# Optimization experiments

Measured on AMD Instinct MI355X. Metric: run time of the kernel, lower is better.

Reference implementation:

```python
import jax, jax.numpy as jnp
import numpy as np

B, TE, TD, EH, DH = 128, 512, 128, 512, 512
K_CNN, C_CNN = 7, 105

def setup_inputs() -> dict:
    key = jax.random.key(0)
    ks = jax.random.split(key, 20)
    n = lambda k, shp: jax.random.normal(k, shp, dtype=jnp.float32) * 0.05
    return {
        "LSTM": jax.random.normal(ks[0], (B, TE, EH), dtype=jnp.float32),
        "CNNs": jax.random.normal(ks[1], (B, K_CNN, C_CNN), dtype=jnp.float32),
        "Wa_w": n(ks[2], (TD, DH)), "Wa_b": n(ks[3], (TD,)),
        "Ua_w": n(ks[4], (TE, EH)), "Ua_b": n(ks[5], (TE,)),
        "va_w": n(ks[6], (1, TE + TD)), "va_b": n(ks[7], (1,)),
        "phi_w": n(ks[8], (EH, TE)), "phi_b": n(ks[9], (EH,)),
        "Wih": n(ks[10], (4 * DH, C_CNN + EH)), "Whh": n(ks[11], (4 * DH, DH)),
        "bih": n(ks[12], (4 * DH,)), "bhh": n(ks[13], (4 * DH,)),
        "wij_w": n(ks[14], (K_CNN, DH + C_CNN)), "wij_b": n(ks[15], (K_CNN,)),
        "s_i": jax.random.uniform(ks[16], (B, DH), dtype=jnp.float32),
        "m_i": jax.random.uniform(ks[17], (B, DH), dtype=jnp.float32),
    }

def reference(LSTM, CNNs, Wa_w, Wa_b, Ua_w, Ua_b, va_w, va_b, phi_w, phi_b,
              Wih, Whh, bih, bhh, wij_w, wij_b, s_i, m_i):
    Bn, Te, Eh = LSTM.shape
    Td = Wa_w.shape[0]
    Dh = s_i.shape[1]
    # delta_i_j for all j: strict lower-triangular one-hots [Te, Te]
    Dm = jnp.tril(jnp.ones((Te, Te), LSTM.dtype), k=-1)
    phi = Dm @ phi_w.T + phi_b                     # [Te, Eh]
    ph = phi[None, :, :] * LSTM                    # [B, Te, Eh] phi_delta * LSTM[:, j]
    Ua = jnp.einsum('bte,se->bts', ph, Ua_w) + Ua_b  # [B, Te, Te]
    Wa = s_i @ Wa_w.T + Wa_b                       # [B, Td] (same for all i, j)
    cat = jnp.concatenate([jnp.broadcast_to(Wa[:, None, :], (Bn, Te, Td)), Ua], axis=-1)
    Cw = jnp.tanh(cat) * va_w[0]                   # [B, Te, Td+Te]
    # one-hot mask picks index i + Te - j; v_a reduces to a single gathered term + bias
    idx = jnp.arange(Td)[:, None] + Te - jnp.arange(Te)[None, :]   # [Td, Te]
    e = Cw[:, jnp.arange(Te)[None, :], idx] + va_b[0]              # [B, Td, Te]
    a = jax.nn.softmax(e, axis=-1)
    c_i = jnp.einsum('bit,bte->bie', a, LSTM)      # [B, Td, Eh]
    # CNN attention (same for all decoder steps; note non-standard normalizer kept faithfully)
    w_cnn, w_s = wij_w[:, :C_CNN], wij_w[:, C_CNN:]
    ep = jnp.tanh(jnp.einsum('bkc,kc->bk', CNNs, w_cnn) + s_i @ w_s.T + wij_b)  # [B, K]
    ap = jnp.exp(ep) / jnp.sum(ep)
    c_p = jnp.einsum('bk,bkc->bc', ap, CNNs)       # [B, C_CNN]
    # LSTMCell with fixed (s_i, m_i) state => all decoder steps vectorize over i
    x = jnp.concatenate([c_i, jnp.broadcast_to(c_p[:, None, :], (Bn, Td, C_CNN))], axis=-1)
    gates = jnp.einsum('bid,gd->big', x, Wih) + bih + (s_i @ Whh.T + bhh)[:, None, :]
    ig, fg, gg, og = jnp.split(gates, 4, axis=-1)
    cnew = jax.nn.sigmoid(fg) * m_i[:, None, :] + jax.nn.sigmoid(ig) * jnp.tanh(gg)
    h = jax.nn.sigmoid(og) * jnp.tanh(cnew)        # [B, Td, Dh]
    return h
```

## Files before the change

kernel.cpp:

```cpp
#include <hip/hip_runtime.h>
#include <hip/hip_bf16.h>

#define B_   128
#define TE_  512
#define TD_  128
#define EH_  512
#define DH_  512
#define KC_  7
#define CC_  105
#define G_   2048
#define KX_  617
#define KP_  640
#define GNT  10

typedef __attribute__((ext_vector_type(8))) short bf16x8;
typedef __attribute__((ext_vector_type(4))) float f32x4;

__device__ __forceinline__ float sigm(float x){ return 1.f/(1.f + __expf(-x)); }
__device__ __forceinline__ float tanhf_fast(float x){
  float e = __expf(2.f*x);
  return 1.f - 2.f/(e + 1.f);
}

__device__ __forceinline__ unsigned short f2bf(float f){
  unsigned int u = __float_as_uint(f);
  unsigned int r = (u + 0x7fffu + ((u >> 16) & 1u)) >> 16;
  return (unsigned short)r;
}

typedef __attribute__((address_space(3))) unsigned int lds_u32_t;
typedef __attribute__((address_space(1))) const unsigned int glb_u32_t;
__device__ __forceinline__ void gload16(const void* g, void* l) {
  __builtin_amdgcn_global_load_lds((glb_u32_t*)g, (lds_u32_t*)l, 16, 0, 0);
}

static const size_t OFF_PHI  = 0;
static const size_t OFF_WA   = OFF_PHI  + (size_t)TE_*EH_*4;
static const size_t OFF_HPRE = OFF_WA   + (size_t)B_*TD_*4;
static const size_t OFF_EP   = OFF_HPRE + (size_t)B_*G_*4;
static const size_t OFF_CP   = OFF_EP   + 4096;
static const size_t OFF_ET   = ((OFF_CP + (size_t)B_*CC_*4 + 255)/256)*256;
static const size_t OFF_STAT = OFF_ET + (size_t)B_*TE_*TD_*4;
static const size_t OFF_P    = ((OFF_STAT + (size_t)2*B_*TD_*4 + 255)/256)*256;
static const size_t OFF_LT   = OFF_P  + (size_t)B_*TD_*TE_*2;
static const size_t OFF_WR   = OFF_LT + (size_t)B_*TE_*EH_*2;
static const size_t OFF_SP   = OFF_WR + (size_t)G_*KP_*2;
static const size_t OFF_PT   = OFF_P;
static const size_t OFF_SUM  = OFF_PT + (size_t)TE_*EH_*4;
static const size_t OFF_WT   = OFF_P + (size_t)2*1024*1024;
static const size_t OFF_WAT  = OFF_P + (size_t)6*1024*1024;

__global__ __launch_bounds__(256) void k_tr(const float* __restrict__ src,
                                            float* __restrict__ dst, int R, int C) {
  int r0 = blockIdx.x * 64, c0 = blockIdx.y * 64;
  __shared__ float tile[64][65];
  int tid = threadIdx.x;
  int r = tid >> 2, c16 = (tid & 3) * 16;
  const float4* s4 = (const float4*)(src + (size_t)(r0 + r)*C + c0 + c16);
  float4 v0 = s4[0], v1 = s4[1], v2 = s4[2], v3 = s4[3];
  *(float4*)&tile[r][c16]    = v0;
  *(float4*)&tile[r][c16+4]  = v1;
  *(float4*)&tile[r][c16+8]  = v2;
  *(float4*)&tile[r][c16+12] = v3;
  __syncthreads();
  float o[16];
  #pragma unroll
  for (int j = 0; j < 16; ++j) o[j] = tile[c16+j][r];
  float* d = dst + (size_t)(c0 + r)*R + r0 + c16;
  *(float4*)d      = *(float4*)&o[0];
  *(float4*)(d+4)  = *(float4*)&o[4];
  *(float4*)(d+8)  = *(float4*)&o[8];
  *(float4*)(d+12) = *(float4*)&o[12];
}

__global__ void k_phiA(const float* __restrict__ phiT, float* __restrict__ phi,
                       float* __restrict__ sums) {
  int e = blockIdx.x * 256 + threadIdx.x;
  int z = blockIdx.y;
  float acc = 0.f;
  for (int t = z*64; t < z*64 + 64; ++t) {
    phi[(size_t)t*EH_ + e] = acc;
    acc += phiT[(size_t)t*EH_ + e];
  }
  sums[z*EH_ + e] = acc;
}
__global__ void k_phiB(const float* __restrict__ sums, const float* __restrict__ phi_b,
                       float* __restrict__ phi) {
  int e = blockIdx.x * 256 + threadIdx.x;
  int z = blockIdx.y;
  float off = phi_b[e];
  for (int zz = 0; zz < z; ++zz) off += sums[zz*EH_ + e];
  for (int t = z*64; t < z*64 + 64; ++t)
    phi[(size_t)t*EH_ + e] += off;
}

__global__ __launch_bounds__(256) void k_wa2(const float* __restrict__ s_i,
                                             const float* __restrict__ WaT,
                                             const float* __restrict__ Wa_b,
                                             const float* __restrict__ va_w,
                                             float* __restrict__ wa) {
  int lane = threadIdx.x & 63, wv = threadIdx.x >> 6;
  int b = blockIdx.x * 4 + wv;
  int d0 = lane * 2;
  const float2* w = (const float2*)WaT + lane;
  const float* s = s_i + (size_t)b*DH_;
  float ax = 0.f, ay = 0.f;
  #pragma unroll 8
  for (int k = 0; k < DH_; ++k) {
    float2 wv2 = w[(size_t)k*64];
    float x = s[k];
    ax += wv2.x * x; ay += wv2.y * x;
  }
  wa[b*TD_ + d0]     = tanhf_fast(ax + Wa_b[d0])     * va_w[d0];
  wa[b*TD_ + d0 + 1] = tanhf_fast(ay + Wa_b[d0 + 1]) * va_w[d0 + 1];
}

__global__ __launch_bounds__(256) void k_hpre2(const float* __restrict__ s_i,
                                               const float* __restrict__ WhhT,
                                               const float* __restrict__ bih,
                                               const float* __restrict__ bhh,
                                               float* __restrict__ hpre) {
  int gq = blockIdx.x * 256 + threadIdx.x;
  int b  = blockIdx.y;
  const float4* w = (const float4*)WhhT + gq;
  const float* s = s_i + (size_t)b*DH_;
  float4 a = {0.f,0.f,0.f,0.f};
  #pragma unroll 8
  for (int k = 0; k < DH_; ++k) {
    float4 wv = w[(size_t)k*512];
    float x = s[k];
    a.x += wv.x*x; a.y += wv.y*x; a.z += wv.z*x; a.w += wv.w*x;
  }
  int g = gq * 4;
  float4 bi = *(const float4*)(bih + g);
  float4 bh = *(const float4*)(bhh + g);
  float4 o;
  o.x = a.x + bi.x + bh.x; o.y = a.y + bi.y + bh.y;
  o.z = a.z + bi.z + bh.z; o.w = a.w + bi.w + bh.w;
  *(float4*)(hpre + (size_t)b*G_ + g) = o;
}

__global__ __launch_bounds__(256) void k_ep(const float* __restrict__ CNNs,
                                            const float* __restrict__ wij_w,
                                            const float* __restrict__ wij_b,
                                            const float* __restrict__ s_i,
                                            float* __restrict__ ep) {
  int gw = blockIdx.x * 4 + (threadIdx.x >> 6);
  int lane = threadIdx.x & 63;
  if (gw >= B_*KC_) return;
  int b = gw / KC_, k = gw % KC_;
  const float* cr = CNNs + (size_t)(b*KC_ + k)*CC_;
  const float* wr = wij_w + (size_t)k*KX_;
  float acc = 0.f;
  for (int c = lane; c < CC_; c += 64) acc += cr[c] * wr[c];
  const float* sr = s_i + (size_t)b*DH_;
  const float* wsr = wr + CC_;
  #pragma unroll
  for (int j = 0; j < 8; ++j) { int h = lane + j*64; acc += sr[h] * wsr[h]; }
  #pragma unroll
  for (int m = 32; m; m >>= 1) acc += __shfl_xor(acc, m, 64);
  if (lane == 0) ep[gw] = tanhf_fast(acc + wij_b[k]);
}

__global__ void k_epsum(const float* __restrict__ ep, float* __restrict__ epsum) {
  __shared__ float red[1024];
  int tid = threadIdx.x;
  red[tid] = (tid < B_*KC_) ? ep[tid] : 0.f;
  __syncthreads();
  for (int off = 512; off > 0; off >>= 1) {
    if (tid < off) red[tid] += red[tid + off];
    __syncthreads();
  }
  if (tid == 0) epsum[0] = red[0];
}

__global__ __launch_bounds__(128) void k_cp(const float* __restrict__ ep,
                                            const float* __restrict__ epsum,
                                            const float* __restrict__ CNNs,
                                            unsigned short* __restrict__ X) {
  int b = blockIdx.x, c = threadIdx.x;
  float S = epsum[0];
  float apl[KC_];
  #pragma unroll
  for (int k = 0; k < KC_; ++k) apl[k] = __expf(ep[b*KC_ + k]) / S;
  float acc = 0.f;
  if (c < CC_) {
    #pragma unroll
    for (int k = 0; k < KC_; ++k)
      acc += apl[k] * CNNs[(size_t)(b*KC_ + k)*CC_ + c];
  }
  unsigned short o = (c < CC_) ? f2bf(acc) : 0;
  unsigned short* xb = X + (size_t)b*TD_*KP_ + EH_ + c;
  for (int i = 0; i < TD_; ++i)
    xb[(size_t)i*KP_] = o;
}

__global__ void k_cvtW(const float* __restrict__ Wih, unsigned short* __restrict__ Wr) {
  int id = blockIdx.x * 256 + threadIdx.x;
  int nr = id / 80, c8 = (id % 80) * 8;
  int gate = nr & 3, dh = nr >> 2;
  const float* src = Wih + (size_t)(gate*DH_ + dh)*KX_;
  unsigned short o[8];
  #pragma unroll
  for (int j = 0; j < 8; ++j) {
    int col = c8 + j;
    o[j] = (col < KX_) ? f2bf(src[col]) : 0;
  }
  *(uint4*)(Wr + (size_t)nr*KP_ + c8) = *(uint4*)o;
}

__global__ __launch_bounds__(256) void k_ltrans(const float* __restrict__ LSTM,
                                                unsigned short* __restrict__ LT) {
  int e0 = blockIdx.x * 64, t0 = blockIdx.y * 64, b = blockIdx.z;
  __shared__ float tile[64][65];
  int tid = threadIdx.x;
  int tt = tid >> 2, c16 = (tid & 3) * 16;
  const float4* src = (const float4*)(LSTM + ((size_t)b*TE_ + t0 + tt)*EH_ + e0 + c16);
  float4 v0 = src[0], v1 = src[1], v2 = src[2], v3 = src[3];
  *(float4*)&tile[tt][c16]    = v0;
  *(float4*)&tile[tt][c16+4]  = v1;
  *(float4*)&tile[tt][c16+8]  = v2;
  *(float4*)&tile[tt][c16+12] = v3;
  __syncthreads();
  int e = tid >> 2, t16 = (tid & 3) * 16;
  unsigned short o[16];
  #pragma unroll
  for (int j = 0; j < 16; ++j) o[j] = f2bf(tile[t16+j][e]);
  unsigned short* dst = LT + ((size_t)b*EH_ + e0 + e)*TE_ + t0 + t16;
  *(uint4*)dst     = *(uint4*)&o[0];
  *(uint4*)(dst+8) = *(uint4*)&o[8];
}

#define BMM_M 64
#define LDA_  40
#define LDB_  40
#define OTS_  132
__global__ __launch_bounds__(256) void k_bandmm(const float* __restrict__ LSTM,
                                                const float* __restrict__ phi,
                                                const float* __restrict__ Ua_w,
                                                const float* __restrict__ Ua_b,
                                                const float* __restrict__ va_w,
                                                const float* __restrict__ va_b,
                                                const float* __restrict__ wa,
                                                unsigned short* __restrict__ P,
                                                float* __restrict__ sums_p) {
  int t0 = blockIdx.x * BMM_M;
  int b  = blockIdx.y;
  int s_base = 321 - t0;
  __shared__ __align__(16) char smem[BMM_M * OTS_ * 4];
  short* sA = (short*)smem;
  short* sB = (short*)(smem + BMM_M*LDA_*2);
  int tid = threadIdx.x;
  int wave = tid >> 6, lane = tid & 63;
  int quad = lane >> 4, l16 = lane & 15;

  f32x4 acc[4][3];
  #pragma unroll
  for (int m = 0; m < 4; ++m)
    #pragma unroll
    for (int n = 0; n < 3; ++n)
      acc[m][n] = (f32x4){0.f, 0.f, 0.f, 0.f};

  int arow = tid >> 2;
  int ach  = (tid & 3) * 8;
  int aq   = ach >> 2;

  const float4* baseL = (const float4*)(LSTM + ((size_t)b*TE_ + t0 + arow)*EH_);
  const float4* baseP = (const float4*)(phi + (size_t)(t0 + arow)*EH_);
  const float4* baseU[3];
  int brow[3], bch[3];
  #pragma unroll
  for (int c = 0; c < 3; ++c) {
    int idx = c*256 + tid;
    brow[c] = idx >> 2;
    bch[c]  = (idx & 3) * 8;
    int s = s_base + brow[c];
    int sc = s < 0 ? 0 : (s > 511 ? 511 : s);
    baseU[c] = (const float4*)(Ua_w + (size_t)sc*EH_ + bch[c]);
  }

  float4 l0 = baseL[aq], l1 = baseL[aq+1], p0 = baseP[aq], p1 = baseP[aq+1];
  float4 u0[3], u1[3];
  #pragma unroll
  for (int c = 0; c < 3; ++c) { u0[c] = baseU[c][0]; u1[c] = baseU[c][1]; }

  for (int k0 = 0; k0 < EH_; k0 += 32) {
    unsigned short at[8];
    at[0]=f2bf(l0.x*p0.x); at[1]=f2bf(l0.y*p0.y); at[2]=f2bf(l0.z*p0.z); at[3]=f2bf(l0.w*p0.w);
    at[4]=f2bf(l1.x*p1.x); at[5]=f2bf(l1.y*p1.y); at[6]=f2bf(l1.z*p1.z); at[7]=f2bf(l1.w*p1.w);
    unsigned short bt[3][8];
    #pragma unroll
    for (int c = 0; c < 3; ++c) {
      bt[c][0]=f2bf(u0[c].x); bt[c][1]=f2bf(u0[c].y); bt[c][2]=f2bf(u0[c].z); bt[c][3]=f2bf(u0[c].w);
      bt[c][4]=f2bf(u1[c].x); bt[c][5]=f2bf(u1[c].y); bt[c][6]=f2bf(u1[c].z); bt[c][7]=f2bf(u1[c].w);
    }
    if (k0 + 32 < EH_) {
      int q = (k0 + 32) >> 2;
      l0 = baseL[q+aq]; l1 = baseL[q+aq+1]; p0 = baseP[q+aq]; p1 = baseP[q+aq+1];
      #pragma unroll
      for (int c = 0; c < 3; ++c) { u0[c] = baseU[c][q]; u1[c] = baseU[c][q+1]; }
    }
    __syncthreads();
    *(uint4*)&sA[arow*LDA_ + ach] = *(uint4*)at;
    #pragma unroll
    for (int c = 0; c < 3; ++c)
      *(uint4*)&sB[brow[c]*LDB_ + bch[c]] = *(uint4*)bt[c];
    __syncthreads();
    bf16x8 bfr[3];
    #pragma unroll
    for (int n = 0; n < 3; ++n)
      bfr[n] = *(const bf16x8*)&sB[(l16 + (wave*3 + n)*16)*LDB_ + quad*8];
    #pragma unroll
    for (int m = 0; m < 4; ++m) {
      bf16x8 af = *(const bf16x8*)&sA[(l16 + m*16)*LDA_ + quad*8];
      #pragma unroll
      for (int n = 0; n < 3; ++n)
        acc[m][n] = __builtin_amdgcn_mfma_f32_16x16x32_bf16(af, bfr[n], acc[m][n], 0, 0, 0);
    }
  }

  __syncthreads();
  float* tileO = (float*)smem;
  float vb = va_b[0];
  #pragma unroll
  for (int n = 0; n < 3; ++n) {
    int s = s_base + wave*48 + n*16 + l16;
    float ub = (s >= 0 && s < TE_) ? Ua_b[s] : 0.f;
    float vw = (s >= 0 && s < TE_) ? va_w[TD_ + s] : 0.f;
    #pragma unroll
    for (int m = 0; m < 4; ++m) {
      #pragma unroll
      for (int r = 0; r < 4; ++r) {
        int tl = m*16 + quad*4 + r;
        int i = s + t0 + tl - 384;
        if (i >= 0 && i < TD_) {
          float val;
          if (s >= 0) val = tanhf_fast(acc[m][n][r] + ub) * vw + vb;
          else        val = wa[b*TD_ + s + 128] + vb;
          tileO[tl*OTS_ + i] = __expf(val);
        }
      }
    }
  }
  __syncthreads();
  if (tid < TD_) {
    float ssum = 0.f;
    #pragma unroll 8
    for (int tl = 0; tl < 64; ++tl) ssum += tileO[tl*OTS_ + tid];
    sums_p[((size_t)b*8 + blockIdx.x)*TD_ + tid] = ssum;
  }
  {
    int ii = tid >> 1, hf = tid & 1;
    unsigned short o[32];
    #pragma unroll
    for (int j = 0; j < 32; ++j)
      o[j] = f2bf(tileO[(hf*32 + j)*OTS_ + ii]);
    unsigned short* dst = P + ((size_t)b*TD_ + ii)*TE_ + t0 + hf*32;
    *(uint4*)dst      = *(uint4*)&o[0];
    *(uint4*)(dst+8)  = *(uint4*)&o[8];
    *(uint4*)(dst+16) = *(uint4*)&o[16];
    *(uint4*)(dst+24) = *(uint4*)&o[24];
  }
}

__global__ __launch_bounds__(128) void k_sinv(const float* __restrict__ sums_p,
                                              float* __restrict__ sinv) {
  int b = blockIdx.x, i = threadIdx.x;
  float s = 0.f;
  #pragma unroll
  for (int z = 0; z < 8; ++z) s += sums_p[((size_t)b*8 + z)*TD_ + i];
  sinv[b*TD_ + i] = 1.f / s;
}

#define CI_LD 40
__global__ __launch_bounds__(256) void k_ci_mm(const unsigned short* __restrict__ P,
                                               const unsigned short* __restrict__ LT,
                                               const float* __restrict__ sinv,
                                               unsigned short* __restrict__ X) {
  int b = blockIdx.x, e0 = blockIdx.y * 128;
  __shared__ short sA[128 * CI_LD];
  __shared__ short sB[128 * CI_LD];
  int tid = threadIdx.x;
  int wave = tid >> 6, lane = tid & 63, quad = lane >> 4, l16 = lane & 15;
  int wm = wave >> 1, wn = wave & 1;
  int row = tid >> 1, ho = (tid & 1) * 16;

  const unsigned short* pa = P + ((size_t)b*TD_ + row)*TE_ + ho;
  const unsigned short* pb = LT + ((size_t)b*EH_ + e0 + row)*TE_ + ho;

  f32x4 acc[4][4];
  #pragma unroll
  for (int m = 0; m < 4; ++m)
    #pragma unroll
    for (int n = 0; n < 4; ++n)
      acc[m][n] = (f32x4){0.f, 0.f, 0.f, 0.f};

  uint4 a0 = *(const uint4*)pa, a1 = *(const uint4*)(pa + 8);
  uint4 b0 = *(const uint4*)pb, b1 = *(const uint4*)(pb + 8);

  for (int k0 = 0; k0 < TE_; k0 += 32) {
    uint4 na0, na1, nb0, nb1;
    if (k0 + 32 < TE_) {
      na0 = *(const uint4*)(pa + k0 + 32); na1 = *(const uint4*)(pa + k0 + 40);
      nb0 = *(const uint4*)(pb + k0 + 32); nb1 = *(const uint4*)(pb + k0 + 40);
    }
    __syncthreads();
    *(uint4*)&sA[row*CI_LD + ho]     = a0;
    *(uint4*)&sA[row*CI_LD + ho + 8] = a1;
    *(uint4*)&sB[row*CI_LD + ho]     = b0;
    *(uint4*)&sB[row*CI_LD + ho + 8] = b1;
    __syncthreads();
    bf16x8 bfr[4];
    #pragma unroll
    for (int n = 0; n < 4; ++n)
      bfr[n] = *(const bf16x8*)&sB[(wn*64 + n*16 + l16)*CI_LD + quad*8];
    #pragma unroll
    for (int m = 0; m < 4; ++m) {
      bf16x8 af = *(const bf16x8*)&sA[(wm*64 + m*16 + l16)*CI_LD + quad*8];
      #pragma unroll
      for (int n = 0; n < 4; ++n)
        acc[m][n] = __builtin_amdgcn_mfma_f32_16x16x32_bf16(af, bfr[n], acc[m][n], 0, 0, 0);
    }
    a0 = na0; a1 = na1; b0 = nb0; b1 = nb1;
  }

  const float* sv = sinv + b*TD_;
  #pragma unroll
  for (int m = 0; m < 4; ++m) {
    int i = wm*64 + m*16 + quad*4;
    float i0 = sv[i], i1 = sv[i+1], i2 = sv[i+2], i3 = sv[i+3];
    #pragma unroll
    for (int n = 0; n < 4; ++n) {
      int e = e0 + wn*64 + n*16 + l16;
      unsigned short* xp = X + ((size_t)b*TD_ + i)*KP_ + e;
      xp[0]              = f2bf(acc[m][n][0] * i0);
      xp[(size_t)KP_]    = f2bf(acc[m][n][1] * i1);
      xp[(size_t)2*KP_]  = f2bf(acc[m][n][2] * i2);
      xp[(size_t)3*KP_]  = f2bf(acc[m][n][3] * i3);
    }
  }
}

__global__ __launch_bounds__(512, 2) void k_gates8(const unsigned short* __restrict__ Wr,
                                                   const unsigned short* __restrict__ X,
                                                   const float* __restrict__ hpre,
                                                   const float* __restrict__ m_i,
                                                   float* __restrict__ out) {
  __shared__ short lds[4 * 256 * 64];
  const int g0  = blockIdx.x * 256;
  const int mi0 = blockIdx.y * 256;
  const int tid  = threadIdx.x;
  const int wave = tid >> 6, lane = tid & 63;
  const int l16 = lane & 15, quad = lane >> 4;
  const int wr = wave >> 2, wc = wave & 3;

  const int srow8 = lane >> 3;
  const int sch   = (lane & 7) ^ srow8;
  const unsigned short* gA = Wr + (size_t)(g0  + wave*8 + srow8) * KP_ + sch*8;
  const unsigned short* gB = X  + (size_t)(mi0 + wave*8 + srow8) * KP_ + sch*8;
  short* lA0 = lds;
  short* lB0 = lds + 16384;
  short* lA1 = lds + 32768;
  short* lB1 = lds + 49152;

  f32x4 acc[8][4];
  #pragma unroll
  for (int m = 0; m < 8; ++m)
    #pragma unroll
    for (int n = 0; n < 4; ++n) acc[m][n] = (f32x4){0.f, 0.f, 0.f, 0.f};

  auto stage = [&](int kt, int bf) {
    short* la = bf ? lA1 : lA0;
    short* lb = bf ? lB1 : lB0;
    const unsigned short* ga = gA + kt*64;
    const unsigned short* gb = gB + kt*64;
    #pragma unroll
    for (int r = 0; r < 4; ++r) {
      gload16(ga + (size_t)r*64*KP_, la + (r*8 + wave)*512);
      gload16(gb + (size_t)r*64*KP_, lb + (r*8 + wave)*512);
    }
  };

  stage(0, 0);
  __syncthreads();

  const int x7 = l16 & 7;
  for (int kt = 0; kt < GNT; ++kt) {
    const int cur = kt & 1;
    if (kt + 1 < GNT) stage(kt + 1, cur ^ 1);
    const short* la = cur ? lA1 : lA0;
    const short* lb = cur ? lB1 : lB0;
    #pragma unroll
    for (int ks = 0; ks < 2; ++ks) {
      const int ck = ((((ks << 2) | quad) ^ x7) << 3);
      bf16x8 bv[4];
      #pragma unroll
      for (int n = 0; n < 4; ++n)
        bv[n] = *(const bf16x8*)&lb[(wc*64 + n*16 + l16)*64 + ck];
      #pragma unroll
      for (int qm = 0; qm < 2; ++qm) {
        bf16x8 av[4];
        #pragma unroll
        for (int m = 0; m < 4; ++m)
          av[m] = *(const bf16x8*)&la[(wr*128 + qm*64 + m*16 + l16)*64 + ck];
        __builtin_amdgcn_s_setprio(1);
        #pragma unroll
        for (int m = 0; m < 4; ++m)
          #pragma unroll
          for (int n = 0; n < 4; ++n)
            acc[qm*4 + m][n] = __builtin_amdgcn_mfma_f32_16x16x32_bf16(av[m], bv[n], acc[qm*4 + m][n], 0, 0, 0);
        __builtin_amdgcn_s_setprio(0);
      }
    }
    __syncthreads();
  }

  const int bb = (mi0 >> 7) + (wc >> 1);
  const float* hp = hpre + (size_t)bb * G_;
  #pragma unroll
  for (int M = 0; M < 8; ++M) {
    const int dh = (g0 >> 2) + wr*32 + M*4 + quad;
    float h0 = hp[dh], h1 = hp[DH_ + dh], h2 = hp[2*DH_ + dh], h3 = hp[3*DH_ + dh];
    float miv = m_i[(size_t)bb*DH_ + dh];
    #pragma unroll
    for (int n = 0; n < 4; ++n) {
      int mi = mi0 + wc*64 + n*16 + l16;
      float ig = acc[M][n][0] + h0;
      float fg = acc[M][n][1] + h1;
      float gg = acc[M][n][2] + h2;
      float og = acc[M][n][3] + h3;
      float c  = sigm(fg)*miv + sigm(ig)*tanhf_fast(gg);
      float h  = sigm(og)*tanhf_fast(c);
      out[(size_t)mi*DH_ + dh] = h;
    }
  }
}

extern "C" void kernel_launch(void* const* d_in, const int* in_sizes, int n_in,
                              void* d_out, int out_size, void* d_ws, size_t ws_size,
                              hipStream_t stream) {
  (void)in_sizes; (void)n_in; (void)out_size; (void)ws_size;
  const float* LSTM  = (const float*)d_in[0];
  const float* CNNs  = (const float*)d_in[1];
  const float* Wa_w  = (const float*)d_in[2];
  const float* Wa_b  = (const float*)d_in[3];
  const float* Ua_w  = (const float*)d_in[4];
  const float* Ua_b  = (const float*)d_in[5];
  const float* va_w  = (const float*)d_in[6];
  const float* va_b  = (const float*)d_in[7];
  const float* phi_w = (const float*)d_in[8];
  const float* phi_b = (const float*)d_in[9];
  const float* Wih   = (const float*)d_in[10];
  const float* Whh   = (const float*)d_in[11];
  const float* bih   = (const float*)d_in[12];
  const float* bhh   = (const float*)d_in[13];
  const float* wij_w = (const float*)d_in[14];
  const float* wij_b = (const float*)d_in[15];
  const float* s_i   = (const float*)d_in[16];
  const float* m_i   = (const float*)d_in[17];
  float* out = (float*)d_out;
  char* ws = (char*)d_ws;

  float* phi  = (float*)(ws + OFF_PHI);
  float* wa   = (float*)(ws + OFF_WA);
  float* hpre = (float*)(ws + OFF_HPRE);
  float* ep   = (float*)(ws + OFF_EP);
  float* epsum= (float*)(ws + OFF_EP) + 1000;
  unsigned short* X  = (unsigned short*)(ws + OFF_ET);
  float* sinv        = (float*)(ws + OFF_STAT);
  unsigned short* P  = (unsigned short*)(ws + OFF_P);
  unsigned short* LT = (unsigned short*)(ws + OFF_LT);
  unsigned short* Wr = (unsigned short*)(ws + OFF_WR);
  float* sums_p      = (float*)(ws + OFF_SP);
  float* phiT        = (float*)(ws + OFF_PT);
  float* sums        = (float*)(ws + OFF_SUM);
  float* WhhT        = (float*)(ws + OFF_WT);
  float* WaT         = (float*)(ws + OFF_WAT);

  k_tr      <<<dim3(8,8),      dim3(256),  0, stream>>>(phi_w, phiT, 512, 512);
  k_tr      <<<dim3(32,8),     dim3(256),  0, stream>>>(Whh, WhhT, 2048, 512);
  k_tr      <<<dim3(2,8),      dim3(256),  0, stream>>>(Wa_w, WaT, 128, 512);
  k_phiA    <<<dim3(2,8),      dim3(256),  0, stream>>>(phiT, phi, sums);
  k_phiB    <<<dim3(2,8),      dim3(256),  0, stream>>>(sums, phi_b, phi);
  k_wa2     <<<dim3(32),       dim3(256),  0, stream>>>(s_i, WaT, Wa_b, va_w, wa);
  k_hpre2   <<<dim3(2,128),    dim3(256),  0, stream>>>(s_i, WhhT, bih, bhh, hpre);
  k_ep      <<<dim3(224),      dim3(256),  0, stream>>>(CNNs, wij_w, wij_b, s_i, ep);
  k_epsum   <<<dim3(1),        dim3(1024), 0, stream>>>(ep, epsum);
  k_cvtW    <<<dim3(640),      dim3(256),  0, stream>>>(Wih, Wr);
  k_ltrans  <<<dim3(8,8,128),  dim3(256),  0, stream>>>(LSTM, LT);
  k_bandmm  <<<dim3(8,128),    dim3(256),  0, stream>>>(LSTM, phi, Ua_w, Ua_b, va_w, va_b, wa, P, sums_p);
  k_sinv    <<<dim3(128),      dim3(128),  0, stream>>>(sums_p, sinv);
  k_cp      <<<dim3(128),      dim3(128),  0, stream>>>(ep, epsum, CNNs, X);
  k_ci_mm   <<<dim3(128,4),    dim3(256),  0, stream>>>(P, LT, sinv, X);
  k_gates8  <<<dim3(8,64),     dim3(512),  0, stream>>>(Wr, X, hpre, m_i, out);
}
```

Measured before the change: 485.5 us.

## Merge sixteen launches into five by fusing prep, mid and post kernels

Several small prep kernels (transposes, Wih conversion, LSTM transpose) are merged into one block-indexed kernel. The phi prefix scan, Wa, hpre and ep computations go into a second fused kernel. The sinv reduction, ep sum and c_p computation are folded into the c_i matmul kernel. This cuts the number of kernel launches and the gaps between them, at the cost of some redundant work: the phi scan recomputes prefix sums serially, and every c_i block with e0==0 re-reduces the full ep array.

New measurement: 504.8 us. +4.0%, slower.

```diff
diff --git a/kernel.cpp b/kernel.cpp
--- a/kernel.cpp
+++ b/kernel.cpp
@@ -46,189 +46,145 @@
 static const size_t OFF_WR   = OFF_LT + (size_t)B_*TE_*EH_*2;
 static const size_t OFF_SP   = OFF_WR + (size_t)G_*KP_*2;
 static const size_t OFF_PT   = OFF_P;
-static const size_t OFF_SUM  = OFF_PT + (size_t)TE_*EH_*4;
 static const size_t OFF_WT   = OFF_P + (size_t)2*1024*1024;
 static const size_t OFF_WAT  = OFF_P + (size_t)6*1024*1024;
 
-__global__ __launch_bounds__(256) void k_tr(const float* __restrict__ src,
-                                            float* __restrict__ dst, int R, int C) {
-  int r0 = blockIdx.x * 64, c0 = blockIdx.y * 64;
+__global__ __launch_bounds__(256) void k_prep(
+    const float* __restrict__ phi_w, float* __restrict__ phiT,
+    const float* __restrict__ Whh,  float* __restrict__ WhhT,
+    const float* __restrict__ Wa_w, float* __restrict__ WaT,
+    const float* __restrict__ Wih,  unsigned short* __restrict__ Wr,
+    const float* __restrict__ LSTM, unsigned short* __restrict__ LT) {
   __shared__ float tile[64][65];
-  int tid = threadIdx.x;
-  int r = tid >> 2, c16 = (tid & 3) * 16;
-  const float4* s4 = (const float4*)(src + (size_t)(r0 + r)*C + c0 + c16);
-  float4 v0 = s4[0], v1 = s4[1], v2 = s4[2], v3 = s4[3];
-  *(float4*)&tile[r][c16]    = v0;
-  *(float4*)&tile[r][c16+4]  = v1;
-  *(float4*)&tile[r][c16+8]  = v2;
-  *(float4*)&tile[r][c16+12] = v3;
-  __syncthreads();
-  float o[16];
-  #pragma unroll
-  for (int j = 0; j < 16; ++j) o[j] = tile[c16+j][r];
-  float* d = dst + (size_t)(c0 + r)*R + r0 + c16;
-  *(float4*)d      = *(float4*)&o[0];
-  *(float4*)(d+4)  = *(float4*)&o[4];
-  *(float4*)(d+8)  = *(float4*)&o[8];
-  *(float4*)(d+12) = *(float4*)&o[12];
-}
-
-__global__ void k_phiA(const float* __restrict__ phiT, float* __restrict__ phi,
-                       float* __restrict__ sums) {
-  int e = blockIdx.x * 256 + threadIdx.x;
-  int z = blockIdx.y;
-  float acc = 0.f;
-  for (int t = z*64; t < z*64 + 64; ++t) {
-    phi[(size_t)t*EH_ + e] = acc;
-    acc += phiT[(size_t)t*EH_ + e];
-  }
-  sums[z*EH_ + e] = acc;
-}
-__global__ void k_phiB(const float* __restrict__ sums, const float* __restrict__ phi_b,
-                       float* __restrict__ phi) {
-  int e = blockIdx.x * 256 + threadIdx.x;
-  int z = blockIdx.y;
-  float off = phi_b[e];
-  for (int zz = 0; zz < z; ++zz) off += sums[zz*EH_ + e];
-  for (int t = z*64; t < z*64 + 64; ++t)
-    phi[(size_t)t*EH_ + e] += off;
-}
-
-__global__ __launch_bounds__(256) void k_wa2(const float* __restrict__ s_i,
-                                             const float* __restrict__ WaT,
-                                             const float* __restrict__ Wa_b,
-                                             const float* __restrict__ va_w,
-                                             float* __restrict__ wa) {
-  int lane = threadIdx.x & 63, wv = threadIdx.x >> 6;
-  int b = blockIdx.x * 4 + wv;
-  int d0 = lane * 2;
-  const float2* w = (const float2*)WaT + lane;
-  const float* s = s_i + (size_t)b*DH_;
-  float ax = 0.f, ay = 0.f;
-  #pragma unroll 8
-  for (int k = 0; k < DH_; ++k) {
-    float2 wv2 = w[(size_t)k*64];
-    float x = s[k];
-    ax += wv2.x * x; ay += wv2.y * x;
-  }
-  wa[b*TD_ + d0]     = tanhf_fast(ax + Wa_b[d0])     * va_w[d0];
-  wa[b*TD_ + d0 + 1] = tanhf_fast(ay + Wa_b[d0 + 1]) * va_w[d0 + 1];
-}
-
-__global__ __launch_bounds__(256) void k_hpre2(const float* __restrict__ s_i,
-                                               const float* __restrict__ WhhT,
-                                               const float* __restrict__ bih,
-                                               const float* __restrict__ bhh,
-                                               float* __restrict__ hpre) {
-  int gq = blockIdx.x * 256 + threadIdx.x;
-  int b  = blockIdx.y;
-  const float4* w = (const float4*)WhhT + gq;
-  const float* s = s_i + (size_t)b*DH_;
-  float4 a = {0.f,0.f,0.f,0.f};
-  #pragma unroll 8
-  for (int k = 0; k < DH_; ++k) {
-    float4 wv = w[(size_t)k*512];
-    float x = s[k];
-    a.x += wv.x*x; a.y += wv.y*x; a.z += wv.z*x; a.w += wv.w*x;
-  }
-  int g = gq * 4;
-  float4 bi = *(const float4*)(bih + g);
-  float4 bh = *(const float4*)(bhh + g);
-  float4 o;
-  o.x = a.x + bi.x + bh.x; o.y = a.y + bi.y + bh.y;
-  o.z = a.z + bi.z + bh.z; o.w = a.w + bi.w + bh.w;
-  *(float4*)(hpre + (size_t)b*G_ + g) = o;
-}
-
-__global__ __launch_bounds__(256) void k_ep(const float* __restrict__ CNNs,
-                                            const float* __restrict__ wij_w,
-                                            const float* __restrict__ wij_b,
-                                            const float* __restrict__ s_i,
-                                            float* __restrict__ ep) {
-  int gw = blockIdx.x * 4 + (threadIdx.x >> 6);
-  int lane = threadIdx.x & 63;
-  if (gw >= B_*KC_) return;
-  int b = gw / KC_, k = gw % KC_;
-  const float* cr = CNNs + (size_t)(b*KC_ + k)*CC_;
-  const float* wr = wij_w + (size_t)k*KX_;
-  float acc = 0.f;
-  for (int c = lane; c < CC_; c += 64) acc += cr[c] * wr[c];
-  const float* sr = s_i + (size_t)b*DH_;
-  const float* wsr = wr + CC_;
-  #pragma unroll
-  for (int j = 0; j < 8; ++j) { int h = lane + j*64; acc += sr[h] * wsr[h]; }
-  #pragma unroll
-  for (int m = 32; m; m >>= 1) acc += __shfl_xor(acc, m, 64);
-  if (lane == 0) ep[gw] = tanhf_fast(acc + wij_b[k]);
-}
-
-__global__ void k_epsum(const float* __restrict__ ep, float* __restrict__ epsum) {
-  __shared__ float red[1024];
-  int tid = threadIdx.x;
-  red[tid] = (tid < B_*KC_) ? ep[tid] : 0.f;
-  __syncthreads();
-  for (int off = 512; off > 0; off >>= 1) {
-    if (tid < off) red[tid] += red[tid + off];
-    __syncthreads();
-  }
-  if (tid == 0) epsum[0] = red[0];
-}
-
-__global__ __launch_bounds__(128) void k_cp(const float* __restrict__ ep,
-                                            const float* __restrict__ epsum,
-                                            const float* __restrict__ CNNs,
-                                            unsigned short* __restrict__ X) {
-  int b = blockIdx.x, c = threadIdx.x;
-  float S = epsum[0];
-  float apl[KC_];
-  #pragma unroll
-  for (int k = 0; k < KC_; ++k) apl[k] = __expf(ep[b*KC_ + k]) / S;
-  float acc = 0.f;
-  if (c < CC_) {
-    #pragma unroll
-    for (int k = 0; k < KC_; ++k)
-      acc += apl[k] * CNNs[(size_t)(b*KC_ + k)*CC_ + c];
-  }
-  unsigned short o = (c < CC_) ? f2bf(acc) : 0;
-  unsigned short* xb = X + (size_t)b*TD_*KP_ + EH_ + c;
-  for (int i = 0; i < TD_; ++i)
-    xb[(size_t)i*KP_] = o;
-}
-
-__global__ void k_cvtW(const float* __restrict__ Wih, unsigned short* __restrict__ Wr) {
-  int id = blockIdx.x * 256 + threadIdx.x;
-  int nr = id / 80, c8 = (id % 80) * 8;
-  int gate = nr & 3, dh = nr >> 2;
-  const float* src = Wih + (size_t)(gate*DH_ + dh)*KX_;
-  unsigned short o[8];
-  #pragma unroll
-  for (int j = 0; j < 8; ++j) {
-    int col = c8 + j;
-    o[j] = (col < KX_) ? f2bf(src[col]) : 0;
-  }
-  *(uint4*)(Wr + (size_t)nr*KP_ + c8) = *(uint4*)o;
-}
-
-__global__ __launch_bounds__(256) void k_ltrans(const float* __restrict__ LSTM,
-                                                unsigned short* __restrict__ LT) {
-  int e0 = blockIdx.x * 64, t0 = blockIdx.y * 64, b = blockIdx.z;
-  __shared__ float tile[64][65];
-  int tid = threadIdx.x;
-  int tt = tid >> 2, c16 = (tid & 3) * 16;
-  const float4* src = (const float4*)(LSTM + ((size_t)b*TE_ + t0 + tt)*EH_ + e0 + c16);
-  float4 v0 = src[0], v1 = src[1], v2 = src[2], v3 = src[3];
-  *(float4*)&tile[tt][c16]    = v0;
-  *(float4*)&tile[tt][c16+4]  = v1;
-  *(float4*)&tile[tt][c16+8]  = v2;
-  *(float4*)&tile[tt][c16+12] = v3;
-  __syncthreads();
-  int e = tid >> 2, t16 = (tid & 3) * 16;
-  unsigned short o[16];
-  #pragma unroll
-  for (int j = 0; j < 16; ++j) o[j] = f2bf(tile[t16+j][e]);
-  unsigned short* dst = LT + ((size_t)b*EH_ + e0 + e)*TE_ + t0 + t16;
-  *(uint4*)dst     = *(uint4*)&o[0];
-  *(uint4*)(dst+8) = *(uint4*)&o[8];
+  int blk = blockIdx.x, tid = threadIdx.x;
+  if (blk < 336) {
+    const float* src; float* dst; int R, i;
+    if (blk < 64)       { src = phi_w; dst = phiT; R = 512;  i = blk; }
+    else if (blk < 320) { src = Whh;   dst = WhhT; R = 2048; i = blk - 64; }
+    else                { src = Wa_w;  dst = WaT;  R = 128;  i = blk - 320; }
+    int nrb = R >> 6;
+    int r0 = (i % nrb) * 64, c0 = (i / nrb) * 64;
+    int r = tid >> 2, c16 = (tid & 3) * 16;
+    const float4* s4 = (const float4*)(src + (size_t)(r0 + r)*512 + c0 + c16);
+    float4 v0 = s4[0], v1 = s4[1], v2 = s4[2], v3 = s4[3];
+    *(float4*)&tile[r][c16]    = v0;
+    *(float4*)&tile[r][c16+4]  = v1;
+    *(float4*)&tile[r][c16+8]  = v2;
+    *(float4*)&tile[r][c16+12] = v3;
+    __syncthreads();
+    float o[16];
+    #pragma unroll
+    for (int j = 0; j < 16; ++j) o[j] = tile[c16+j][r];
+    float* d = dst + (size_t)(c0 + r)*R + r0 + c16;
+    *(float4*)d      = *(float4*)&o[0];
+    *(float4*)(d+4)  = *(float4*)&o[4];
+    *(float4*)(d+8)  = *(float4*)&o[8];
+    *(float4*)(d+12) = *(float4*)&o[12];
+  } else if (blk < 976) {
+    int id = (blk - 336) * 256 + tid;
+    int nr = id / 80, c8 = (id % 80) * 8;
+    int gate = nr & 3, dh = nr >> 2;
+    const float* src = Wih + (size_t)(gate*DH_ + dh)*KX_;
+    unsigned short o[8];
+    #pragma unroll
+    for (int j = 0; j < 8; ++j) {
+      int col = c8 + j;
+      o[j] = (col < KX_) ? f2bf(src[col]) : 0;
+    }
+    *(uint4*)(Wr + (size_t)nr*KP_ + c8) = *(uint4*)o;
+  } else {
+    int i = blk - 976;
+    int e0 = (i & 7) * 64, t0 = ((i >> 3) & 7) * 64, b = i >> 6;
+    int tt = tid >> 2, c16 = (tid & 3) * 16;
+    const float4* src = (const float4*)(LSTM + ((size_t)b*TE_ + t0 + tt)*EH_ + e0 + c16);
+    float4 v0 = src[0], v1 = src[1], v2 = src[2], v3 = src[3];
+    *(float4*)&tile[tt][c16]    = v0;
+    *(float4*)&tile[tt][c16+4]  = v1;
+    *(float4*)&tile[tt][c16+8]  = v2;
+    *(float4*)&tile[tt][c16+12] = v3;
+    __syncthreads();
+    int e = tid >> 2, t16 = (tid & 3) * 16;
+    unsigned short o[16];
+    #pragma unroll
+    for (int j = 0; j < 16; ++j) o[j] = f2bf(tile[t16+j][e]);
+    unsigned short* dst = LT + ((size_t)b*EH_ + e0 + e)*TE_ + t0 + t16;
+    *(uint4*)dst     = *(uint4*)&o[0];
+    *(uint4*)(dst+8) = *(uint4*)&o[8];
+  }
+}
+
+__global__ __launch_bounds__(256) void k_mid(
+    const float* __restrict__ phiT, const float* __restrict__ phi_b, float* __restrict__ phi,
+    const float* __restrict__ WaT, const float* __restrict__ Wa_b,
+    const float* __restrict__ va_w, float* __restrict__ wa,
+    const float* __restrict__ WhhT, const float* __restrict__ bih,
+    const float* __restrict__ bhh, float* __restrict__ hpre,
+    const float* __restrict__ CNNs, const float* __restrict__ wij_w,
+    const float* __restrict__ wij_b,
+    const float* __restrict__ s_i, float* __restrict__ ep) {
+  int blk = blockIdx.x, tid = threadIdx.x;
+  if (blk < 16) {
+    int e = (blk & 1) * 256 + tid;
+    int z = blk >> 1;
+    float off = phi_b[e];
+    for (int t = 0; t < z*64; ++t) off += phiT[(size_t)t*EH_ + e];
+    for (int t = z*64; t < z*64 + 64; ++t) {
+      phi[(size_t)t*EH_ + e] = off;
+      off += phiT[(size_t)t*EH_ + e];
+    }
+  } else if (blk < 48) {
+    int lane = tid & 63, wv = tid >> 6;
+    int b = (blk - 16) * 4 + wv;
+    int d0 = lane * 2;
+    const float2* w = (const float2*)WaT + lane;
+    const float* s = s_i + (size_t)b*DH_;
+    float ax = 0.f, ay = 0.f;
+    #pragma unroll 8
+    for (int k = 0; k < DH_; ++k) {
+      float2 wv2 = w[(size_t)k*64];
+      float x = s[k];
+      ax += wv2.x * x; ay += wv2.y * x;
+    }
+    wa[b*TD_ + d0]     = tanhf_fast(ax + Wa_b[d0])     * va_w[d0];
+    wa[b*TD_ + d0 + 1] = tanhf_fast(ay + Wa_b[d0 + 1]) * va_w[d0 + 1];
+  } else if (blk < 304) {
+    int i = blk - 48;
+    int gq = (i & 1) * 256 + tid;
+    int b  = i >> 1;
+    const float4* w = (const float4*)WhhT + gq;
+    const float* s = s_i + (size_t)b*DH_;
+    float4 a = {0.f,0.f,0.f,0.f};
+    #pragma unroll 8
+    for (int k = 0; k < DH_; ++k) {
+      float4 wv = w[(size_t)k*512];
+      float x = s[k];
+      a.x += wv.x*x; a.y += wv.y*x; a.z += wv.z*x; a.w += wv.w*x;
+    }
+    int g = gq * 4;
+    float4 bi = *(const float4*)(bih + g);
+    float4 bh = *(const float4*)(bhh + g);
+    float4 o;
+    o.x = a.x + bi.x + bh.x; o.y = a.y + bi.y + bh.y;
+    o.z = a.z + bi.z + bh.z; o.w = a.w + bi.w + bh.w;
+    *(float4*)(hpre + (size_t)b*G_ + g) = o;
+  } else {
+    int gw = (blk - 304) * 4 + (tid >> 6);
+    int lane = tid & 63;
+    if (gw < B_*KC_) {
+      int b = gw / KC_, k = gw % KC_;
+      const float* cr = CNNs + (size_t)(b*KC_ + k)*CC_;
+      const float* wr = wij_w + (size_t)k*KX_;
+      float acc = 0.f;
+      for (int c = lane; c < CC_; c += 64) acc += cr[c] * wr[c];
+      const float* sr = s_i + (size_t)b*DH_;
+      const float* wsr = wr + CC_;
+      #pragma unroll
+      for (int j = 0; j < 8; ++j) { int h = lane + j*64; acc += sr[h] * wsr[h]; }
+      #pragma unroll
+      for (int m = 32; m; m >>= 1) acc += __shfl_xor(acc, m, 64);
+      if (lane == 0) ep[gw] = tanhf_fast(acc + wij_b[k]);
+    }
+  }
 }
 
 #define BMM_M 64
@@ -363,27 +319,29 @@
   }
 }
 
-__global__ __launch_bounds__(128) void k_sinv(const float* __restrict__ sums_p,
-                                              float* __restrict__ sinv) {
-  int b = blockIdx.x, i = threadIdx.x;
-  float s = 0.f;
-  #pragma unroll
-  for (int z = 0; z < 8; ++z) s += sums_p[((size_t)b*8 + z)*TD_ + i];
-  sinv[b*TD_ + i] = 1.f / s;
-}
-
 #define CI_LD 40
-__global__ __launch_bounds__(256) void k_ci_mm(const unsigned short* __restrict__ P,
-                                               const unsigned short* __restrict__ LT,
-                                               const float* __restrict__ sinv,
-                                               unsigned short* __restrict__ X) {
+__global__ __launch_bounds__(256) void k_ci2(const unsigned short* __restrict__ P,
+                                             const unsigned short* __restrict__ LT,
+                                             const float* __restrict__ sums_p,
+                                             const float* __restrict__ ep,
+                                             const float* __restrict__ CNNs,
+                                             unsigned short* __restrict__ X) {
   int b = blockIdx.x, e0 = blockIdx.y * 128;
   __shared__ short sA[128 * CI_LD];
   __shared__ short sB[128 * CI_LD];
+  __shared__ float svL[TD_];
+  __shared__ float red2[256];
   int tid = threadIdx.x;
   int wave = tid >> 6, lane = tid & 63, quad = lane >> 4, l16 = lane & 15;
   int wm = wave >> 1, wn = wave & 1;
   int row = tid >> 1, ho = (tid & 1) * 16;
+
+  if (tid < TD_) {
+    float s = 0.f;
+    #pragma unroll
+    for (int z = 0; z < 8; ++z) s += sums_p[((size_t)b*8 + z)*TD_ + tid];
+    svL[tid] = 1.f / s;
+  }
 
   const unsigned short* pa = P + ((size_t)b*TD_ + row)*TE_ + ho;
   const unsigned short* pb = LT + ((size_t)b*EH_ + e0 + row)*TE_ + ho;
@@ -424,11 +382,10 @@
     a0 = na0; a1 = na1; b0 = nb0; b1 = nb1;
   }
 
-  const float* sv = sinv + b*TD_;
   #pragma unroll
   for (int m = 0; m < 4; ++m) {
     int i = wm*64 + m*16 + quad*4;
-    float i0 = sv[i], i1 = sv[i+1], i2 = sv[i+2], i3 = sv[i+3];
+    float i0 = svL[i], i1 = svL[i+1], i2 = svL[i+2], i3 = svL[i+3];
     #pragma unroll
     for (int n = 0; n < 4; ++n) {
       int e = e0 + wn*64 + n*16 + l16;
@@ -437,6 +394,35 @@
       xp[(size_t)KP_]    = f2bf(acc[m][n][1] * i1);
       xp[(size_t)2*KP_]  = f2bf(acc[m][n][2] * i2);
       xp[(size_t)3*KP_]  = f2bf(acc[m][n][3] * i3);
+    }
+  }
+
+  if (e0 == 0) {
+    __syncthreads();
+    float p = 0.f;
+    for (int j = tid; j < B_*KC_; j += 256) p += ep[j];
+    red2[tid] = p;
+    __syncthreads();
+    for (int off = 128; off > 0; off >>= 1) {
+      if (tid < off) red2[tid] += red2[tid + off];
+      __syncthreads();
+    }
+    float S = red2[0];
+    int c = tid;
+    if (c < 128) {
+      float apl[KC_];
+      #pragma unroll
+      for (int k = 0; k < KC_; ++k) apl[k] = __expf(ep[b*KC_ + k]) / S;
+      float acc2 = 0.f;
+      if (c < CC_) {
+        #pragma unroll
+        for (int k = 0; k < KC_; ++k)
+          acc2 += apl[k] * CNNs[(size_t)(b*KC_ + k)*CC_ + c];
+      }
+      unsigned short o = (c < CC_) ? f2bf(acc2) : 0;
+      unsigned short* xb = X + (size_t)b*TD_*KP_ + EH_ + c;
+      for (int i = 0; i < TD_; ++i)
+        xb[(size_t)i*KP_] = o;
     }
   }
 }
@@ -565,32 +551,23 @@
   float* wa   = (float*)(ws + OFF_WA);
   float* hpre = (float*)(ws + OFF_HPRE);
   float* ep   = (float*)(ws + OFF_EP);
-  float* epsum= (float*)(ws + OFF_EP) + 1000;
   unsigned short* X  = (unsigned short*)(ws + OFF_ET);
-  float* sinv        = (float*)(ws + OFF_STAT);
   unsigned short* P  = (unsigned short*)(ws + OFF_P);
   unsigned short* LT = (unsigned short*)(ws + OFF_LT);
   unsigned short* Wr = (unsigned short*)(ws + OFF_WR);
   float* sums_p      = (float*)(ws + OFF_SP);
   float* phiT        = (float*)(ws + OFF_PT);
-  float* sums        = (float*)(ws + OFF_SUM);
   float* WhhT        = (float*)(ws + OFF_WT);
   float* WaT         = (float*)(ws + OFF_WAT);
 
-  k_tr      <<<dim3(8,8),      dim3(256),  0, stream>>>(phi_w, phiT, 512, 512);
-  k_tr      <<<dim3(32,8),     dim3(256),  0, stream>>>(Whh, WhhT, 2048, 512);
-  k_tr      <<<dim3(2,8),      dim3(256),  0, stream>>>(Wa_w, WaT, 128, 512);
-  k_phiA    <<<dim3(2,8),      dim3(256),  0, stream>>>(phiT, phi, sums);
-  k_phiB    <<<dim3(2,8),      dim3(256),  0, stream>>>(sums, phi_b, phi);
-  k_wa2     <<<dim3(32),       dim3(256),  0, stream>>>(s_i, WaT, Wa_b, va_w, wa);
-  k_hpre2   <<<dim3(2,128),    dim3(256),  0, stream>>>(s_i, WhhT, bih, bhh, hpre);
-  k_ep      <<<dim3(224),      dim3(256),  0, stream>>>(CNNs, wij_w, wij_b, s_i, ep);
-  k_epsum   <<<dim3(1),        dim3(1024), 0, stream>>>(ep, epsum);
-  k_cvtW    <<<dim3(640),      dim3(256),  0, stream>>>(Wih, Wr);
-  k_ltrans  <<<dim3(8,8,128),  dim3(256),  0, stream>>>(LSTM, LT);
-  k_bandmm  <<<dim3(8,128),    dim3(256),  0, stream>>>(LSTM, phi, Ua_w, Ua_b, va_w, va_b, wa, P, sums_p);
-  k_sinv    <<<dim3(128),      dim3(128),  0, stream>>>(sums_p, sinv);
-  k_cp      <<<dim3(128),      dim3(128),  0, stream>>>(ep, epsum, CNNs, X);
-  k_ci_mm   <<<dim3(128,4),    dim3(256),  0, stream>>>(P, LT, sinv, X);
-  k_gates8  <<<dim3(8,64),     dim3(512),  0, stream>>>(Wr, X, hpre, m_i, out);
-}
+  k_prep  <<<dim3(9168),  dim3(256), 0, stream>>>(phi_w, phiT, Whh, WhhT, Wa_w, WaT,
+                                                  Wih, Wr, LSTM, LT);
+  k_mid   <<<dim3(528),   dim3(256), 0, stream>>>(phiT, phi_b, phi,
+                                                  WaT, Wa_b, va_w, wa,
+                                                  WhhT, bih, bhh, hpre,
+                                                  CNNs, wij_w, wij_b, s_i, ep);
+  k_bandmm<<<dim3(8,128), dim3(256), 0, stream>>>(LSTM, phi, Ua_w, Ua_b, va_w, va_b,
+                                                  wa, P, sums_p);
+  k_ci2   <<<dim3(128,4), dim3(256), 0, stream>>>(P, LT, sums_p, ep, CNNs, X);
+  k_gates8<<<dim3(8,64),  dim3(512), 0, stream>>>(Wr, X, hpre, m_i, out);
+}
```
